# Kernel optimization log

Hardware: AMD Instinct MI355X
Metric: run time of the kernel (lower is better)

Reference implementation:

```python
import jax, jax.numpy as jnp
import numpy as np

D = 256        # node/edge feature dim
H = 256        # MLP hidden dim
NG = 80000     # grid (src) nodes
NM = 20000     # mesh (dst) nodes
E = 160000     # g2m edges
EPS = 1e-5


def _mlp(x, W1, b1, W2, b2, g, beta):
    # MeshGraphMLP with hidden_layers=1: Linear -> SiLU -> Linear -> LayerNorm
    h = jax.nn.silu(x @ W1 + b1)
    y = h @ W2 + b2
    mu = jnp.mean(y, axis=-1, keepdims=True)
    var = jnp.var(y, axis=-1, keepdims=True)
    return (y - mu) * jax.lax.rsqrt(var + EPS) * g + beta


def setup_inputs() -> dict:
    key = jax.random.key(0)
    ks = jax.random.split(key, 16)

    def rn(k, shape, s=0.02):
        return jax.random.normal(k, shape, dtype=jnp.float32) * s

    inp = {
        "g2m_efeat": jax.random.normal(ks[0], (E, D), dtype=jnp.float32),
        "grid_nfeat": jax.random.normal(ks[1], (NG, D), dtype=jnp.float32),
        "mesh_nfeat": jax.random.normal(ks[2], (NM, D), dtype=jnp.float32),
        "src_idx": jax.random.randint(ks[3], (E,), 0, NG, dtype=jnp.int32),
        "dst_idx": jax.random.randint(ks[4], (E,), 0, NM, dtype=jnp.int32),
        # edge MLP (concat variant): input = [efeat | src_feat | dst_feat] -> 3D
        "eW1": rn(ks[5], (3 * D, H)), "eb1": jnp.zeros((H,), jnp.float32),
        "eW2": rn(ks[6], (H, D)),     "eb2": jnp.zeros((D,), jnp.float32),
        "eg": jnp.ones((D,), jnp.float32), "ebeta": jnp.zeros((D,), jnp.float32),
        # src node MLP: D -> H -> D
        "sW1": rn(ks[7], (D, H)), "sb1": jnp.zeros((H,), jnp.float32),
        "sW2": rn(ks[8], (H, D)), "sb2": jnp.zeros((D,), jnp.float32),
        "sg": jnp.ones((D,), jnp.float32), "sbeta": jnp.zeros((D,), jnp.float32),
        # dst node MLP: (D_agg + D_node) = 2D -> H -> D
        "dW1": rn(ks[9], (2 * D, H)), "db1": jnp.zeros((H,), jnp.float32),
        "dW2": rn(ks[10], (H, D)),    "db2": jnp.zeros((D,), jnp.float32),
        "dg": jnp.ones((D,), jnp.float32), "dbeta": jnp.zeros((D,), jnp.float32),
    }
    return inp


def reference(g2m_efeat, grid_nfeat, mesh_nfeat, src_idx, dst_idx,
              eW1, eb1, eW2, eb2, eg, ebeta,
              sW1, sb1, sW2, sb2, sg, sbeta,
              dW1, db1, dW2, db2, dg, dbeta):
    # edge MLP: gather src/dst node features, concat with edge features
    e_in = jnp.concatenate(
        [g2m_efeat, grid_nfeat[src_idx], mesh_nfeat[dst_idx]], axis=-1)  # [E, 3D]
    efeat = _mlp(e_in, eW1, eb1, eW2, eb2, eg, ebeta)                    # [E, D]
    # aggregate_and_concat: copy_e_sum scatter to dst mesh nodes, concat node feats
    agg = jax.ops.segment_sum(efeat, dst_idx, num_segments=NM)           # [NM, D]
    cat_feat = jnp.concatenate([agg, mesh_nfeat], axis=-1)               # [NM, 2D]
    mesh_out = mesh_nfeat + _mlp(cat_feat, dW1, db1, dW2, db2, dg, dbeta)
    grid_out = grid_nfeat + _mlp(grid_nfeat, sW1, sb1, sW2, sb2, sg, sbeta)
    return (grid_out, mesh_out)
```

## Files before the change

kernel.cpp:

```cpp
#include <hip/hip_runtime.h>
#include <hip/hip_bf16.h>

#define DD 256
#define NGN 80000
#define NMN 20000
#define NEE 160000

typedef unsigned short u16;
typedef __attribute__((ext_vector_type(8))) short s16x8;
typedef __attribute__((ext_vector_type(4))) short s16x4;
typedef __attribute__((ext_vector_type(4))) float f32x4;

__device__ __forceinline__ u16 f2bf(float f) {
  union { float f; unsigned u; } v; v.f = f;
  unsigned r = (v.u + 0x7FFFu + ((v.u >> 16) & 1u)) >> 16;
  return (u16)r;
}
__device__ __forceinline__ float bf2f(u16 x) {
  union { unsigned u; float f; } v; v.u = ((unsigned)x) << 16;
  return v.f;
}

__global__ void pack_weights(const float* __restrict__ W, u16* __restrict__ dst, int K) {
  int idx = blockIdx.x * 256 + threadIdx.x;
  if (idx >= K * 256) return;
  int i = idx & 7;
  int lane = (idx >> 3) & 63;
  int nt = (idx >> 9) & 15;
  int kt = idx >> 13;
  int k = kt * 32 + 4 * (lane >> 4) + (i < 4 ? i : 12 + i);
  int n = nt * 16 + (lane & 15);
  dst[idx] = f2bf(W[(size_t)k * 256 + n]);
}

__device__ __forceinline__ void stage16k(const u16* __restrict__ gsrc, u16* lds, int tid) {
  const s16x8* s = (const s16x8*)gsrc;
  s16x8* d = (s16x8*)lds;
#pragma unroll
  for (int j = 0; j < 4; ++j) d[tid + 256 * j] = s[tid + 256 * j];
}

__global__ __launch_bounds__(256, 2) void gemm_ns(
    const float* __restrict__ X, const u16* __restrict__ Wp,
    u16* __restrict__ Y, int n) {
  __shared__ u16 bstage[8192];
  __shared__ u16 ob[16384];
  const int tid = threadIdx.x;
  const int lane = tid & 63;
  const int wave = tid >> 6;
  const int mr = wave >> 1, nc = wave & 1;
  const int g = lane >> 4, lr = lane & 15;
  const int row0 = blockIdx.x * 64;

  const float* pX[2];
#pragma unroll
  for (int mt = 0; mt < 2; ++mt) {
    int r = min(row0 + mr * 32 + mt * 16 + lr, n - 1);
    pX[mt] = X + (size_t)r * DD;
  }
  const f32x4 fz = {0.f, 0.f, 0.f, 0.f};
  f32x4 acc[2][8];
#pragma unroll
  for (int mt = 0; mt < 2; ++mt)
#pragma unroll
    for (int nt = 0; nt < 8; ++nt) acc[mt][nt] = fz;

  for (int kl = 0; kl < 8; ++kl) {
    __syncthreads();
    stage16k(Wp + (size_t)kl * 8192, bstage, tid);
    __syncthreads();
    s16x8 afr[2];
    const int c0 = kl * 32 + 4 * g;
#pragma unroll
    for (int mt = 0; mt < 2; ++mt) {
      f32x4 f0 = *(const f32x4*)(pX[mt] + c0);
      f32x4 f1 = *(const f32x4*)(pX[mt] + c0 + 16);
      s16x8 a;
#pragma unroll
      for (int j = 0; j < 4; ++j) {
        a[j] = (short)f2bf(f0[j]);
        a[4 + j] = (short)f2bf(f1[j]);
      }
      afr[mt] = a;
    }
#pragma unroll
    for (int nt = 0; nt < 8; ++nt) {
      s16x8 b = *(const s16x8*)(bstage + ((size_t)(nc * 8 + nt) * 64 + lane) * 8);
      acc[0][nt] = __builtin_amdgcn_mfma_f32_16x16x32_bf16(afr[0], b, acc[0][nt], 0, 0, 0);
      acc[1][nt] = __builtin_amdgcn_mfma_f32_16x16x32_bf16(afr[1], b, acc[1][nt], 0, 0, 0);
    }
  }
#pragma unroll
  for (int mt = 0; mt < 2; ++mt)
#pragma unroll
    for (int nt = 0; nt < 8; ++nt)
#pragma unroll
      for (int i = 0; i < 4; ++i) {
        int rowL = mr * 32 + mt * 16 + 4 * g + i;
        int col = nc * 128 + nt * 16 + lr;
        int byte = rowL * 512 + ((col * 2) ^ ((rowL & 7) << 4));
        *(u16*)((char*)ob + byte) = f2bf(acc[mt][nt][i]);
      }
  __syncthreads();
#pragma unroll
  for (int rr = 0; rr < 16; ++rr) {
    int rowL = wave * 16 + rr;
    int rg = row0 + rowL;
    if (rg < n) {
      s16x4 v = *(const s16x4*)((char*)ob + rowL * 512 + ((lane * 8) ^ ((rowL & 7) << 4)));
      *(s16x4*)(Y + (size_t)rg * DD + lane * 4) = v;
    }
  }
}

__global__ __launch_bounds__(256, 2) void edge_fused(
    const float* __restrict__ efeat,
    const u16* __restrict__ GSp, const u16* __restrict__ GMp,
    const int* __restrict__ sidx, const int* __restrict__ didx,
    const u16* __restrict__ W1p, const float* __restrict__ b1,
    const u16* __restrict__ W2p, const float* __restrict__ b2,
    const float* __restrict__ gam, const float* __restrict__ bet,
    float* __restrict__ agg) {
  __shared__ u16 uni[16384];
  __shared__ u16 bstage[8192];
  __shared__ float2 pstats[64][2];

  const int tid = threadIdx.x;
  const int lane = tid & 63;
  const int wave = tid >> 6;
  const int mr = wave >> 1, nc = wave & 1;
  const int g = lane >> 4, lr = lane & 15;
  const int row0 = blockIdx.x * 64;

#pragma unroll
  for (int j = 0; j < 8; ++j) {
    int e = wave * 16 + j * 2 + (lane >> 5);
    int rg = row0 + e;
    int rs = sidx[rg], rd = didx[rg];
    int co = (lane & 31) * 8;
    s16x8 a = *(const s16x8*)(GSp + (size_t)rs * DD + co);
    s16x8 b = *(const s16x8*)(GMp + (size_t)rd * DD + co);
    s16x8 o;
#pragma unroll
    for (int k2 = 0; k2 < 8; ++k2)
      o[k2] = (short)f2bf(bf2f((u16)a[k2]) + bf2f((u16)b[k2]));
    int byte = e * 512 + ((co * 2) ^ ((e & 7) << 4));
    *(s16x8*)((char*)uni + byte) = o;
  }
  __syncthreads();

  f32x4 acc[2][8];
#pragma unroll
  for (int mt = 0; mt < 2; ++mt)
#pragma unroll
    for (int nt = 0; nt < 8; ++nt)
#pragma unroll
      for (int i = 0; i < 4; ++i) {
        int rowL = mr * 32 + mt * 16 + 4 * g + i;
        int col = nc * 128 + nt * 16 + lr;
        int byte = rowL * 512 + ((col * 2) ^ ((rowL & 7) << 4));
        acc[mt][nt][i] = bf2f(*(const u16*)((char*)uni + byte));
      }

  const float* pe[2];
#pragma unroll
  for (int mt = 0; mt < 2; ++mt)
    pe[mt] = efeat + (size_t)(row0 + mr * 32 + mt * 16 + lr) * DD;

  for (int kl = 0; kl < 8; ++kl) {
    __syncthreads();
    stage16k(W1p + (size_t)kl * 8192, bstage, tid);
    __syncthreads();
    s16x8 afr[2];
    const int c0 = kl * 32 + 4 * g;
#pragma unroll
    for (int mt = 0; mt < 2; ++mt) {
      f32x4 f0 = *(const f32x4*)(pe[mt] + c0);
      f32x4 f1 = *(const f32x4*)(pe[mt] + c0 + 16);
      s16x8 a;
#pragma unroll
      for (int j = 0; j < 4; ++j) {
        a[j] = (short)f2bf(f0[j]);
        a[4 + j] = (short)f2bf(f1[j]);
      }
      afr[mt] = a;
    }
#pragma unroll
    for (int nt = 0; nt < 8; ++nt) {
      s16x8 b = *(const s16x8*)(bstage + ((size_t)(nc * 8 + nt) * 64 + lane) * 8);
      acc[0][nt] = __builtin_amdgcn_mfma_f32_16x16x32_bf16(afr[0], b, acc[0][nt], 0, 0, 0);
      acc[1][nt] = __builtin_amdgcn_mfma_f32_16x16x32_bf16(afr[1], b, acc[1][nt], 0, 0, 0);
    }
  }

  {
    float b1v[8];
#pragma unroll
    for (int nt = 0; nt < 8; ++nt) b1v[nt] = b1[nc * 128 + nt * 16 + lr];
#pragma unroll
    for (int mt = 0; mt < 2; ++mt)
#pragma unroll
      for (int nt = 0; nt < 8; ++nt)
#pragma unroll
        for (int i = 0; i < 4; ++i) {
          float x = acc[mt][nt][i] + b1v[nt];
          float h = x / (1.f + __expf(-x));
          int rowL = mr * 32 + mt * 16 + 4 * g + i;
          int col = nc * 128 + nt * 16 + lr;
          int byte = rowL * 512 + ((col * 2) ^ ((rowL & 7) << 4));
          *(u16*)((char*)uni + byte) = f2bf(h);
        }
  }

  f32x4 acc2[2][8];
  const f32x4 fz = {0.f, 0.f, 0.f, 0.f};
#pragma unroll
  for (int mt = 0; mt < 2; ++mt)
#pragma unroll
    for (int nt = 0; nt < 8; ++nt) acc2[mt][nt] = fz;

  for (int kt2 = 0; kt2 < 8; ++kt2) {
    __syncthreads();
    stage16k(W2p + (size_t)kt2 * 8192, bstage, tid);
    __syncthreads();
    s16x8 afr[2];
#pragma unroll
    for (int mt = 0; mt < 2; ++mt) {
      int rowL = mr * 32 + mt * 16 + lr;
      int swz = (rowL & 7) << 4;
      int cL = kt2 * 32 + 4 * g;
      s16x4 lo = *(const s16x4*)((char*)uni + rowL * 512 + ((cL * 2) ^ swz));
      s16x4 hi = *(const s16x4*)((char*)uni + rowL * 512 + (((cL + 16) * 2) ^ swz));
      s16x8 a;
#pragma unroll
      for (int j = 0; j < 4; ++j) {
        a[j] = lo[j];
        a[4 + j] = hi[j];
      }
      afr[mt] = a;
    }
#pragma unroll
    for (int nt = 0; nt < 8; ++nt) {
      s16x8 b = *(const s16x8*)(bstage + ((size_t)(nc * 8 + nt) * 64 + lane) * 8);
      acc2[0][nt] = __builtin_amdgcn_mfma_f32_16x16x32_bf16(afr[0], b, acc2[0][nt], 0, 0, 0);
      acc2[1][nt] = __builtin_amdgcn_mfma_f32_16x16x32_bf16(afr[1], b, acc2[1][nt], 0, 0, 0);
    }
  }

  float b2v[8], gv[8], bv[8];
#pragma unroll
  for (int nt = 0; nt < 8; ++nt) {
    int col = nc * 128 + nt * 16 + lr;
    b2v[nt] = b2[col];
    gv[nt] = gam[col];
    bv[nt] = bet[col];
  }
#pragma unroll
  for (int mt = 0; mt < 2; ++mt)
#pragma unroll
    for (int i = 0; i < 4; ++i) {
      float s = 0.f, s2 = 0.f;
#pragma unroll
      for (int nt = 0; nt < 8; ++nt) {
        float y = acc2[mt][nt][i] + b2v[nt];
        s += y;
        s2 += y * y;
      }
#pragma unroll
      for (int m = 1; m < 16; m <<= 1) {
        s += __shfl_xor(s, m);
        s2 += __shfl_xor(s2, m);
      }
      if (lr == 0) pstats[mr * 32 + mt * 16 + 4 * g + i][nc] = make_float2(s, s2);
    }
  __syncthreads();
#pragma unroll
  for (int mt = 0; mt < 2; ++mt)
#pragma unroll
    for (int i = 0; i < 4; ++i) {
      int rowL = mr * 32 + mt * 16 + 4 * g + i;
      float2 pa = pstats[rowL][0], pb = pstats[rowL][1];
      float sum = pa.x + pb.x, sq = pa.y + pb.y;
      float mu = sum * (1.f / 256.f);
      float var = fmaxf(sq * (1.f / 256.f) - mu * mu, 0.f);
      float rs = rsqrtf(var + 1e-5f);
      int rg = row0 + rowL;
      int dn = didx[rg];
#pragma unroll
      for (int nt = 0; nt < 8; ++nt) {
        int col = nc * 128 + nt * 16 + lr;
        float y = acc2[mt][nt][i] + b2v[nt];
        float val = (y - mu) * rs * gv[nt] + bv[nt];
        atomicAdd(agg + (size_t)dn * DD + col, val);
      }
    }
}

template <int MODE, int K1>
__global__ __launch_bounds__(256, 2) void mlp_fused(
    const float* __restrict__ xa, const float* __restrict__ xb,
    const u16* __restrict__ W1p, const float* __restrict__ b1,
    const u16* __restrict__ W2p, const float* __restrict__ b2,
    const float* __restrict__ gam, const float* __restrict__ bet,
    const float* __restrict__ resid, float* __restrict__ out, int nrows) {
  __shared__ u16 bstage[8192];
  __shared__ u16 hbuf[64 * 256];
  __shared__ float2 pstats[64][2];

  const int tid = threadIdx.x;
  const int lane = tid & 63;
  const int wave = tid >> 6;
  const int mr = wave >> 1, nc = wave & 1;
  const int g = lane >> 4, lr = lane & 15;
  const int row0 = blockIdx.x * 64;

  const float* pA[2][2];
#pragma unroll
  for (int mt = 0; mt < 2; ++mt) {
    int r = row0 + mr * 32 + mt * 16 + lr;
    if (MODE == 2) r = min(r, nrows - 1);
    pA[mt][0] = xa + (size_t)r * DD;
    if constexpr (MODE == 2) pA[mt][1] = xb + (size_t)r * DD;
  }

  const f32x4 fz = {0.f, 0.f, 0.f, 0.f};
  f32x4 acc[2][8];
#pragma unroll
  for (int mt = 0; mt < 2; ++mt)
#pragma unroll
    for (int nt = 0; nt < 8; ++nt) acc[mt][nt] = fz;

#pragma unroll
  for (int region = 0; region < K1 / 256; ++region) {
    for (int kl = 0; kl < 8; ++kl) {
      const int kt = region * 8 + kl;
      __syncthreads();
      stage16k(W1p + (size_t)kt * 8192, bstage, tid);
      __syncthreads();
      s16x8 afr[2];
      const int c0 = kl * 32 + 4 * g;
#pragma unroll
      for (int mt = 0; mt < 2; ++mt) {
        const float* p = pA[mt][region] + c0;
        f32x4 f0 = *(const f32x4*)p;
        f32x4 f1 = *(const f32x4*)(p + 16);
        s16x8 a;
#pragma unroll
        for (int j = 0; j < 4; ++j) {
          a[j] = (short)f2bf(f0[j]);
          a[4 + j] = (short)f2bf(f1[j]);
        }
        afr[mt] = a;
      }
#pragma unroll
      for (int nt = 0; nt < 8; ++nt) {
        s16x8 b = *(const s16x8*)(bstage + ((size_t)(nc * 8 + nt) * 64 + lane) * 8);
        acc[0][nt] = __builtin_amdgcn_mfma_f32_16x16x32_bf16(afr[0], b, acc[0][nt], 0, 0, 0);
        acc[1][nt] = __builtin_amdgcn_mfma_f32_16x16x32_bf16(afr[1], b, acc[1][nt], 0, 0, 0);
      }
    }
  }

  {
    float b1v[8];
#pragma unroll
    for (int nt = 0; nt < 8; ++nt) b1v[nt] = b1[nc * 128 + nt * 16 + lr];
#pragma unroll
    for (int mt = 0; mt < 2; ++mt)
#pragma unroll
      for (int nt = 0; nt < 8; ++nt)
#pragma unroll
        for (int i = 0; i < 4; ++i) {
          float x = acc[mt][nt][i] + b1v[nt];
          float h = x / (1.f + __expf(-x));
          int rowL = mr * 32 + mt * 16 + 4 * g + i;
          int col = nc * 128 + nt * 16 + lr;
          int byte = rowL * 512 + ((col * 2) ^ ((rowL & 7) << 4));
          *(u16*)((char*)hbuf + byte) = f2bf(h);
        }
  }

  f32x4 acc2[2][8];
#pragma unroll
  for (int mt = 0; mt < 2; ++mt)
#pragma unroll
    for (int nt = 0; nt < 8; ++nt) acc2[mt][nt] = fz;

  for (int kt2 = 0; kt2 < 8; ++kt2) {
    __syncthreads();
    stage16k(W2p + (size_t)kt2 * 8192, bstage, tid);
    __syncthreads();
    s16x8 afr[2];
#pragma unroll
    for (int mt = 0; mt < 2; ++mt) {
      int rowL = mr * 32 + mt * 16 + lr;
      int swz = (rowL & 7) << 4;
      int cL = kt2 * 32 + 4 * g;
      s16x4 lo = *(const s16x4*)((char*)hbuf + rowL * 512 + ((cL * 2) ^ swz));
      s16x4 hi = *(const s16x4*)((char*)hbuf + rowL * 512 + (((cL + 16) * 2) ^ swz));
      s16x8 a;
#pragma unroll
      for (int j = 0; j < 4; ++j) {
        a[j] = lo[j];
        a[4 + j] = hi[j];
      }
      afr[mt] = a;
    }
#pragma unroll
    for (int nt = 0; nt < 8; ++nt) {
      s16x8 b = *(const s16x8*)(bstage + ((size_t)(nc * 8 + nt) * 64 + lane) * 8);
      acc2[0][nt] = __builtin_amdgcn_mfma_f32_16x16x32_bf16(afr[0], b, acc2[0][nt], 0, 0, 0);
      acc2[1][nt] = __builtin_amdgcn_mfma_f32_16x16x32_bf16(afr[1], b, acc2[1][nt], 0, 0, 0);
    }
  }

  float b2v[8], gv[8], bv[8];
#pragma unroll
  for (int nt = 0; nt < 8; ++nt) {
    int col = nc * 128 + nt * 16 + lr;
    b2v[nt] = b2[col];
    gv[nt] = gam[col];
    bv[nt] = bet[col];
  }
#pragma unroll
  for (int mt = 0; mt < 2; ++mt)
#pragma unroll
    for (int i = 0; i < 4; ++i) {
      float s = 0.f, s2 = 0.f;
#pragma unroll
      for (int nt = 0; nt < 8; ++nt) {
        float y = acc2[mt][nt][i] + b2v[nt];
        s += y;
        s2 += y * y;
      }
#pragma unroll
      for (int m = 1; m < 16; m <<= 1) {
        s += __shfl_xor(s, m);
        s2 += __shfl_xor(s2, m);
      }
      if (lr == 0) pstats[mr * 32 + mt * 16 + 4 * g + i][nc] = make_float2(s, s2);
    }
  __syncthreads();
#pragma unroll
  for (int mt = 0; mt < 2; ++mt)
#pragma unroll
    for (int i = 0; i < 4; ++i) {
      int rowL = mr * 32 + mt * 16 + 4 * g + i;
      float2 pa = pstats[rowL][0], pb = pstats[rowL][1];
      float sum = pa.x + pb.x, sq = pa.y + pb.y;
      float mu = sum * (1.f / 256.f);
      float var = fmaxf(sq * (1.f / 256.f) - mu * mu, 0.f);
      float rs = rsqrtf(var + 1e-5f);
      int rg = row0 + rowL;
      if (MODE == 2 && rg >= nrows) continue;
#pragma unroll
      for (int nt = 0; nt < 8; ++nt) {
        int col = nc * 128 + nt * 16 + lr;
        float y = acc2[mt][nt][i] + b2v[nt];
        float val = (y - mu) * rs * gv[nt] + bv[nt];
        out[(size_t)rg * DD + col] = resid[(size_t)rg * DD + col] + val;
      }
    }
}

extern "C" void kernel_launch(void* const* d_in, const int* in_sizes, int n_in,
                              void* d_out, int out_size, void* d_ws, size_t ws_size,
                              hipStream_t stream) {
  const float* g2m  = (const float*)d_in[0];
  const float* grid = (const float*)d_in[1];
  const float* mesh = (const float*)d_in[2];
  const int* sidx = (const int*)d_in[3];
  const int* didx = (const int*)d_in[4];
  const float* eW1 = (const float*)d_in[5];
  const float* eb1 = (const float*)d_in[6];
  const float* eW2 = (const float*)d_in[7];
  const float* eb2 = (const float*)d_in[8];
  const float* eg  = (const float*)d_in[9];
  const float* ebt = (const float*)d_in[10];
  const float* sW1 = (const float*)d_in[11];
  const float* sb1 = (const float*)d_in[12];
  const float* sW2 = (const float*)d_in[13];
  const float* sb2 = (const float*)d_in[14];
  const float* sg  = (const float*)d_in[15];
  const float* sbt = (const float*)d_in[16];
  const float* dW1 = (const float*)d_in[17];
  const float* db1 = (const float*)d_in[18];
  const float* dW2 = (const float*)d_in[19];
  const float* db2 = (const float*)d_in[20];
  const float* dg  = (const float*)d_in[21];
  const float* dbt = (const float*)d_in[22];

  float* agg = (float*)d_ws;
  u16* wp = (u16*)((char*)d_ws + (size_t)NMN * DD * 4);
  u16* eW1p = wp;
  u16* eW2p = eW1p + 768 * 256;
  u16* sW1p = eW2p + 256 * 256;
  u16* sW2p = sW1p + 256 * 256;
  u16* dW1p = sW2p + 256 * 256;
  u16* dW2p = dW1p + 512 * 256;

  float* gout = (float*)d_out;
  float* mout = gout + (size_t)NGN * DD;
  u16* GSp = (u16*)d_out;
  u16* GMp = GSp + (size_t)NGN * DD;

  (void)hipMemsetAsync(agg, 0, (size_t)NMN * DD * 4, stream);
  pack_weights<<<768, 256, 0, stream>>>(eW1, eW1p, 768);
  pack_weights<<<256, 256, 0, stream>>>(eW2, eW2p, 256);
  pack_weights<<<256, 256, 0, stream>>>(sW1, sW1p, 256);
  pack_weights<<<256, 256, 0, stream>>>(sW2, sW2p, 256);
  pack_weights<<<512, 256, 0, stream>>>(dW1, dW1p, 512);
  pack_weights<<<256, 256, 0, stream>>>(dW2, dW2p, 256);

  gemm_ns<<<NGN / 64, 256, 0, stream>>>(grid, eW1p + 8 * 8192, GSp, NGN);
  gemm_ns<<<(NMN + 63) / 64, 256, 0, stream>>>(mesh, eW1p + 16 * 8192, GMp, NMN);

  edge_fused<<<NEE / 64, 256, 0, stream>>>(
      g2m, GSp, GMp, sidx, didx, eW1p, eb1, eW2p, eb2, eg, ebt, agg);

  mlp_fused<2, 512><<<(NMN + 63) / 64, 256, 0, stream>>>(
      agg, mesh, dW1p, db1, dW2p, db2, dg, dbt, mesh, mout, NMN);
  mlp_fused<1, 256><<<NGN / 64, 256, 0, stream>>>(
      grid, nullptr, sW1p, sb1, sW2p, sb2, sg, sbt, grid, gout, NGN);
}
```

Baseline: 446.9 us.

## Sort edges by destination via CSR and segment-reduce before atomics; drop weight LDS staging

Builds a destination-sorted edge permutation (histogram, scan, fill) so each edge block processes edges grouped by destination and reduces consecutive same-destination rows in LDS before issuing one atomicAdd per run, instead of one atomic per edge element. Weight B-fragments are now read directly from global memory rather than staged through LDS with per-k barriers. The A operands are staged once into swizzled LDS as bf16, and launch bounds rise to 4 blocks per CU. The trade-offs are three extra small kernels, the gather of efeat through the permutation, and B traffic that now depends on cache hits.

```diff
diff --git a/kernel.cpp b/kernel.cpp
--- a/kernel.cpp
+++ b/kernel.cpp
@@ -33,18 +33,50 @@
   dst[idx] = f2bf(W[(size_t)k * 256 + n]);
 }
 
-__device__ __forceinline__ void stage16k(const u16* __restrict__ gsrc, u16* lds, int tid) {
-  const s16x8* s = (const s16x8*)gsrc;
-  s16x8* d = (s16x8*)lds;
-#pragma unroll
-  for (int j = 0; j < 4; ++j) d[tid + 256 * j] = s[tid + 256 * j];
-}
-
-__global__ __launch_bounds__(256, 2) void gemm_ns(
+__global__ void csr_hist(const int* __restrict__ didx, int* __restrict__ cnt) {
+  int i = blockIdx.x * 256 + threadIdx.x;
+  if (i < NEE) atomicAdd(cnt + didx[i], 1);
+}
+__global__ void csr_scan(const int* __restrict__ cnt, int* __restrict__ cursor) {
+  __shared__ int psum[256];
+  const int CH = (NMN + 255) / 256;
+  int t = threadIdx.x;
+  int base = t * CH, s = 0;
+  for (int k = 0; k < CH; ++k) { int i = base + k; if (i < NMN) s += cnt[i]; }
+  psum[t] = s;
+  __syncthreads();
+  for (int off = 1; off < 256; off <<= 1) {
+    int v = (t >= off) ? psum[t - off] : 0;
+    __syncthreads();
+    psum[t] += v;
+    __syncthreads();
+  }
+  int run = psum[t] - s;
+  for (int k = 0; k < CH; ++k) {
+    int i = base + k;
+    if (i < NMN) { cursor[i] = run; run += cnt[i]; }
+  }
+}
+__global__ void csr_fill(const int* __restrict__ didx, int* __restrict__ cursor,
+                         int* __restrict__ eids) {
+  int e = blockIdx.x * 256 + threadIdx.x;
+  if (e < NEE) { int p = atomicAdd(cursor + didx[e], 1); eids[p] = e; }
+}
+
+__device__ __forceinline__ s16x8 ldsA(const u16* uni, int rowL, int cL) {
+  int swz = (rowL & 7) << 4;
+  s16x4 lo = *(const s16x4*)((const char*)uni + rowL * 512 + ((cL * 2) ^ swz));
+  s16x4 hi = *(const s16x4*)((const char*)uni + rowL * 512 + (((cL + 16) * 2) ^ swz));
+  s16x8 a;
+#pragma unroll
+  for (int j = 0; j < 4; ++j) { a[j] = lo[j]; a[4 + j] = hi[j]; }
+  return a;
+}
+
+__global__ __launch_bounds__(256, 4) void gemm_ns(
     const float* __restrict__ X, const u16* __restrict__ Wp,
     u16* __restrict__ Y, int n) {
-  __shared__ u16 bstage[8192];
-  __shared__ u16 ob[16384];
+  __shared__ u16 uni[16384];
   const int tid = threadIdx.x;
   const int lane = tid & 63;
   const int wave = tid >> 6;
@@ -52,12 +84,21 @@
   const int g = lane >> 4, lr = lane & 15;
   const int row0 = blockIdx.x * 64;
 
-  const float* pX[2];
-#pragma unroll
-  for (int mt = 0; mt < 2; ++mt) {
-    int r = min(row0 + mr * 32 + mt * 16 + lr, n - 1);
-    pX[mt] = X + (size_t)r * DD;
-  }
+#pragma unroll
+  for (int j = 0; j < 8; ++j) {
+    int e = wave * 16 + j * 2 + (lane >> 5);
+    int r = min(row0 + e, n - 1);
+    const float* src = X + (size_t)r * DD + (lane & 31) * 8;
+    f32x4 f0 = *(const f32x4*)src;
+    f32x4 f1 = *(const f32x4*)(src + 4);
+    s16x8 o;
+#pragma unroll
+    for (int k = 0; k < 4; ++k) { o[k] = (short)f2bf(f0[k]); o[4 + k] = (short)f2bf(f1[k]); }
+    int co = (lane & 31) * 8;
+    *(s16x8*)((char*)uni + e * 512 + ((co * 2) ^ ((e & 7) << 4))) = o;
+  }
+  __syncthreads();
+
   const f32x4 fz = {0.f, 0.f, 0.f, 0.f};
   f32x4 acc[2][8];
 #pragma unroll
@@ -66,30 +107,23 @@
     for (int nt = 0; nt < 8; ++nt) acc[mt][nt] = fz;
 
   for (int kl = 0; kl < 8; ++kl) {
-    __syncthreads();
-    stage16k(Wp + (size_t)kl * 8192, bstage, tid);
-    __syncthreads();
     s16x8 afr[2];
-    const int c0 = kl * 32 + 4 * g;
-#pragma unroll
-    for (int mt = 0; mt < 2; ++mt) {
-      f32x4 f0 = *(const f32x4*)(pX[mt] + c0);
-      f32x4 f1 = *(const f32x4*)(pX[mt] + c0 + 16);
-      s16x8 a;
-#pragma unroll
-      for (int j = 0; j < 4; ++j) {
-        a[j] = (short)f2bf(f0[j]);
-        a[4 + j] = (short)f2bf(f1[j]);
-      }
-      afr[mt] = a;
-    }
-#pragma unroll
-    for (int nt = 0; nt < 8; ++nt) {
-      s16x8 b = *(const s16x8*)(bstage + ((size_t)(nc * 8 + nt) * 64 + lane) * 8);
-      acc[0][nt] = __builtin_amdgcn_mfma_f32_16x16x32_bf16(afr[0], b, acc[0][nt], 0, 0, 0);
-      acc[1][nt] = __builtin_amdgcn_mfma_f32_16x16x32_bf16(afr[1], b, acc[1][nt], 0, 0, 0);
-    }
-  }
+#pragma unroll
+    for (int mt = 0; mt < 2; ++mt) afr[mt] = ldsA(uni, mr * 32 + mt * 16 + lr, kl * 32 + 4 * g);
+#pragma unroll
+    for (int h = 0; h < 2; ++h) {
+      s16x8 bfr[4];
+#pragma unroll
+      for (int q = 0; q < 4; ++q)
+        bfr[q] = *(const s16x8*)(Wp + (size_t)kl * 8192 + ((nc * 8 + h * 4 + q) * 64 + lane) * 8);
+#pragma unroll
+      for (int q = 0; q < 4; ++q) {
+        acc[0][h * 4 + q] = __builtin_amdgcn_mfma_f32_16x16x32_bf16(afr[0], bfr[q], acc[0][h * 4 + q], 0, 0, 0);
+        acc[1][h * 4 + q] = __builtin_amdgcn_mfma_f32_16x16x32_bf16(afr[1], bfr[q], acc[1][h * 4 + q], 0, 0, 0);
+      }
+    }
+  }
+  __syncthreads();
 #pragma unroll
   for (int mt = 0; mt < 2; ++mt)
 #pragma unroll
@@ -98,8 +132,7 @@
       for (int i = 0; i < 4; ++i) {
         int rowL = mr * 32 + mt * 16 + 4 * g + i;
         int col = nc * 128 + nt * 16 + lr;
-        int byte = rowL * 512 + ((col * 2) ^ ((rowL & 7) << 4));
-        *(u16*)((char*)ob + byte) = f2bf(acc[mt][nt][i]);
+        *(u16*)((char*)uni + rowL * 512 + ((col * 2) ^ ((rowL & 7) << 4))) = f2bf(acc[mt][nt][i]);
       }
   __syncthreads();
 #pragma unroll
@@ -107,23 +140,25 @@
     int rowL = wave * 16 + rr;
     int rg = row0 + rowL;
     if (rg < n) {
-      s16x4 v = *(const s16x4*)((char*)ob + rowL * 512 + ((lane * 8) ^ ((rowL & 7) << 4)));
+      s16x4 v = *(const s16x4*)((char*)uni + rowL * 512 + ((lane * 8) ^ ((rowL & 7) << 4)));
       *(s16x4*)(Y + (size_t)rg * DD + lane * 4) = v;
     }
   }
 }
 
-__global__ __launch_bounds__(256, 2) void edge_fused(
+__global__ __launch_bounds__(256, 4) void edge_fused(
     const float* __restrict__ efeat,
     const u16* __restrict__ GSp, const u16* __restrict__ GMp,
-    const int* __restrict__ sidx, const int* __restrict__ didx,
+    const int* __restrict__ sidx, const int* __restrict__ eids,
     const u16* __restrict__ W1p, const float* __restrict__ b1,
     const u16* __restrict__ W2p, const float* __restrict__ b2,
     const float* __restrict__ gam, const float* __restrict__ bet,
-    float* __restrict__ agg) {
+    const int* __restrict__ didx, float* __restrict__ agg) {
   __shared__ u16 uni[16384];
-  __shared__ u16 bstage[8192];
   __shared__ float2 pstats[64][2];
+  __shared__ int eidL[64];
+  __shared__ int srcL[64];
+  __shared__ int dstL[64];
 
   const int tid = threadIdx.x;
   const int lane = tid & 63;
@@ -132,20 +167,24 @@
   const int g = lane >> 4, lr = lane & 15;
   const int row0 = blockIdx.x * 64;
 
+  if (tid < 64) {
+    int e = eids[row0 + tid];
+    eidL[tid] = e;
+    srcL[tid] = sidx[e];
+    dstL[tid] = didx[e];
+  }
+  __syncthreads();
+
 #pragma unroll
   for (int j = 0; j < 8; ++j) {
     int e = wave * 16 + j * 2 + (lane >> 5);
-    int rg = row0 + e;
-    int rs = sidx[rg], rd = didx[rg];
     int co = (lane & 31) * 8;
-    s16x8 a = *(const s16x8*)(GSp + (size_t)rs * DD + co);
-    s16x8 b = *(const s16x8*)(GMp + (size_t)rd * DD + co);
+    s16x8 a = *(const s16x8*)(GSp + (size_t)srcL[e] * DD + co);
+    s16x8 b = *(const s16x8*)(GMp + (size_t)dstL[e] * DD + co);
     s16x8 o;
 #pragma unroll
-    for (int k2 = 0; k2 < 8; ++k2)
-      o[k2] = (short)f2bf(bf2f((u16)a[k2]) + bf2f((u16)b[k2]));
-    int byte = e * 512 + ((co * 2) ^ ((e & 7) << 4));
-    *(s16x8*)((char*)uni + byte) = o;
+    for (int k = 0; k < 8; ++k) o[k] = (short)f2bf(bf2f((u16)a[k]) + bf2f((u16)b[k]));
+    *(s16x8*)((char*)uni + e * 512 + ((co * 2) ^ ((e & 7) << 4))) = o;
   }
   __syncthreads();
 
@@ -158,40 +197,42 @@
       for (int i = 0; i < 4; ++i) {
         int rowL = mr * 32 + mt * 16 + 4 * g + i;
         int col = nc * 128 + nt * 16 + lr;
-        int byte = rowL * 512 + ((col * 2) ^ ((rowL & 7) << 4));
-        acc[mt][nt][i] = bf2f(*(const u16*)((char*)uni + byte));
-      }
-
-  const float* pe[2];
-#pragma unroll
-  for (int mt = 0; mt < 2; ++mt)
-    pe[mt] = efeat + (size_t)(row0 + mr * 32 + mt * 16 + lr) * DD;
+        acc[mt][nt][i] = bf2f(*(const u16*)((char*)uni + rowL * 512 + ((col * 2) ^ ((rowL & 7) << 4))));
+      }
+  __syncthreads();
+
+#pragma unroll
+  for (int j = 0; j < 8; ++j) {
+    int e = wave * 16 + j * 2 + (lane >> 5);
+    const float* src = efeat + (size_t)eidL[e] * DD + (lane & 31) * 8;
+    f32x4 f0 = *(const f32x4*)src;
+    f32x4 f1 = *(const f32x4*)(src + 4);
+    s16x8 o;
+#pragma unroll
+    for (int k = 0; k < 4; ++k) { o[k] = (short)f2bf(f0[k]); o[4 + k] = (short)f2bf(f1[k]); }
+    int co = (lane & 31) * 8;
+    *(s16x8*)((char*)uni + e * 512 + ((co * 2) ^ ((e & 7) << 4))) = o;
+  }
+  __syncthreads();
 
   for (int kl = 0; kl < 8; ++kl) {
-    __syncthreads();
-    stage16k(W1p + (size_t)kl * 8192, bstage, tid);
-    __syncthreads();
     s16x8 afr[2];
-    const int c0 = kl * 32 + 4 * g;
-#pragma unroll
-    for (int mt = 0; mt < 2; ++mt) {
-      f32x4 f0 = *(const f32x4*)(pe[mt] + c0);
-      f32x4 f1 = *(const f32x4*)(pe[mt] + c0 + 16);
-      s16x8 a;
-#pragma unroll
-      for (int j = 0; j < 4; ++j) {
-        a[j] = (short)f2bf(f0[j]);
-        a[4 + j] = (short)f2bf(f1[j]);
-      }
-      afr[mt] = a;
-    }
-#pragma unroll
-    for (int nt = 0; nt < 8; ++nt) {
-      s16x8 b = *(const s16x8*)(bstage + ((size_t)(nc * 8 + nt) * 64 + lane) * 8);
-      acc[0][nt] = __builtin_amdgcn_mfma_f32_16x16x32_bf16(afr[0], b, acc[0][nt], 0, 0, 0);
-      acc[1][nt] = __builtin_amdgcn_mfma_f32_16x16x32_bf16(afr[1], b, acc[1][nt], 0, 0, 0);
-    }
-  }
+#pragma unroll
+    for (int mt = 0; mt < 2; ++mt) afr[mt] = ldsA(uni, mr * 32 + mt * 16 + lr, kl * 32 + 4 * g);
+#pragma unroll
+    for (int h = 0; h < 2; ++h) {
+      s16x8 bfr[4];
+#pragma unroll
+      for (int q = 0; q < 4; ++q)
+        bfr[q] = *(const s16x8*)(W1p + (size_t)kl * 8192 + ((nc * 8 + h * 4 + q) * 64 + lane) * 8);
+#pragma unroll
+      for (int q = 0; q < 4; ++q) {
+        acc[0][h * 4 + q] = __builtin_amdgcn_mfma_f32_16x16x32_bf16(afr[0], bfr[q], acc[0][h * 4 + q], 0, 0, 0);
+        acc[1][h * 4 + q] = __builtin_amdgcn_mfma_f32_16x16x32_bf16(afr[1], bfr[q], acc[1][h * 4 + q], 0, 0, 0);
+      }
+    }
+  }
+  __syncthreads();
 
   {
     float b1v[8];
@@ -207,10 +248,10 @@
           float h = x / (1.f + __expf(-x));
           int rowL = mr * 32 + mt * 16 + 4 * g + i;
           int col = nc * 128 + nt * 16 + lr;
-          int byte = rowL * 512 + ((col * 2) ^ ((rowL & 7) << 4));
-          *(u16*)((char*)uni + byte) = f2bf(h);
+          *(u16*)((char*)uni + rowL * 512 + ((col * 2) ^ ((rowL & 7) << 4))) = f2bf(h);
         }
   }
+  __syncthreads();
 
   f32x4 acc2[2][8];
   const f32x4 fz = {0.f, 0.f, 0.f, 0.f};
@@ -218,32 +259,21 @@
   for (int mt = 0; mt < 2; ++mt)
 #pragma unroll
     for (int nt = 0; nt < 8; ++nt) acc2[mt][nt] = fz;
-
-  for (int kt2 = 0; kt2 < 8; ++kt2) {
-    __syncthreads();
-    stage16k(W2p + (size_t)kt2 * 8192, bstage, tid);
-    __syncthreads();
+  for (int kl = 0; kl < 8; ++kl) {
     s16x8 afr[2];
 #pragma unroll
-    for (int mt = 0; mt < 2; ++mt) {
-      int rowL = mr * 32 + mt * 16 + lr;
-      int swz = (rowL & 7) << 4;
-      int cL = kt2 * 32 + 4 * g;
-      s16x4 lo = *(const s16x4*)((char*)uni + rowL * 512 + ((cL * 2) ^ swz));
-      s16x4 hi = *(const s16x4*)((char*)uni + rowL * 512 + (((cL + 16) * 2) ^ swz));
-      s16x8 a;
-#pragma unroll
-      for (int j = 0; j < 4; ++j) {
-        a[j] = lo[j];
-        a[4 + j] = hi[j];
-      }
-      afr[mt] = a;
-    }
-#pragma unroll
-    for (int nt = 0; nt < 8; ++nt) {
-      s16x8 b = *(const s16x8*)(bstage + ((size_t)(nc * 8 + nt) * 64 + lane) * 8);
-      acc2[0][nt] = __builtin_amdgcn_mfma_f32_16x16x32_bf16(afr[0], b, acc2[0][nt], 0, 0, 0);
-      acc2[1][nt] = __builtin_amdgcn_mfma_f32_16x16x32_bf16(afr[1], b, acc2[1][nt], 0, 0, 0);
+    for (int mt = 0; mt < 2; ++mt) afr[mt] = ldsA(uni, mr * 32 + mt * 16 + lr, kl * 32 + 4 * g);
+#pragma unroll
+    for (int h = 0; h < 2; ++h) {
+      s16x8 bfr[4];
+#pragma unroll
+      for (int q = 0; q < 4; ++q)
+        bfr[q] = *(const s16x8*)(W2p + (size_t)kl * 8192 + ((nc * 8 + h * 4 + q) * 64 + lane) * 8);
+#pragma unroll
+      for (int q = 0; q < 4; ++q) {
+        acc2[0][h * 4 + q] = __builtin_amdgcn_mfma_f32_16x16x32_bf16(afr[0], bfr[q], acc2[0][h * 4 + q], 0, 0, 0);
+        acc2[1][h * 4 + q] = __builtin_amdgcn_mfma_f32_16x16x32_bf16(afr[1], bfr[q], acc2[1][h * 4 + q], 0, 0, 0);
+      }
     }
   }
 
@@ -274,6 +304,7 @@
       if (lr == 0) pstats[mr * 32 + mt * 16 + 4 * g + i][nc] = make_float2(s, s2);
     }
   __syncthreads();
+
 #pragma unroll
   for (int mt = 0; mt < 2; ++mt)
 #pragma unroll
@@ -284,27 +315,42 @@
       float mu = sum * (1.f / 256.f);
       float var = fmaxf(sq * (1.f / 256.f) - mu * mu, 0.f);
       float rs = rsqrtf(var + 1e-5f);
-      int rg = row0 + rowL;
-      int dn = didx[rg];
 #pragma unroll
       for (int nt = 0; nt < 8; ++nt) {
         int col = nc * 128 + nt * 16 + lr;
         float y = acc2[mt][nt][i] + b2v[nt];
         float val = (y - mu) * rs * gv[nt] + bv[nt];
-        atomicAdd(agg + (size_t)dn * DD + col, val);
-      }
-    }
+        *(u16*)((char*)uni + rowL * 512 + ((col * 2) ^ ((rowL & 7) << 4))) = f2bf(val);
+      }
+    }
+  __syncthreads();
+
+  {
+    int c = tid;
+    float sum = 0.f;
+    int prev = dstL[0];
+#pragma unroll 8
+    for (int r = 0; r < 64; ++r) {
+      int d = dstL[r];
+      if (d != prev) {
+        atomicAdd(agg + (size_t)prev * DD + c, sum);
+        sum = 0.f;
+        prev = d;
+      }
+      sum += bf2f(*(const u16*)((char*)uni + r * 512 + ((c * 2) ^ ((r & 7) << 4))));
+    }
+    atomicAdd(agg + (size_t)prev * DD + c, sum);
+  }
 }
 
 template <int MODE, int K1>
-__global__ __launch_bounds__(256, 2) void mlp_fused(
+__global__ __launch_bounds__(256, 4) void mlp_fused(
     const float* __restrict__ xa, const float* __restrict__ xb,
     const u16* __restrict__ W1p, const float* __restrict__ b1,
     const u16* __restrict__ W2p, const float* __restrict__ b2,
     const float* __restrict__ gam, const float* __restrict__ bet,
     const float* __restrict__ resid, float* __restrict__ out, int nrows) {
-  __shared__ u16 bstage[8192];
-  __shared__ u16 hbuf[64 * 256];
+  __shared__ u16 uni[16384];
   __shared__ float2 pstats[64][2];
 
   const int tid = threadIdx.x;
@@ -314,15 +360,6 @@
   const int g = lane >> 4, lr = lane & 15;
   const int row0 = blockIdx.x * 64;
 
-  const float* pA[2][2];
-#pragma unroll
-  for (int mt = 0; mt < 2; ++mt) {
-    int r = row0 + mr * 32 + mt * 16 + lr;
-    if (MODE == 2) r = min(r, nrows - 1);
-    pA[mt][0] = xa + (size_t)r * DD;
-    if constexpr (MODE == 2) pA[mt][1] = xb + (size_t)r * DD;
-  }
-
   const f32x4 fz = {0.f, 0.f, 0.f, 0.f};
   f32x4 acc[2][8];
 #pragma unroll
@@ -332,34 +369,42 @@
 
 #pragma unroll
   for (int region = 0; region < K1 / 256; ++region) {
+    __syncthreads();
+    const float* Xr = (region == 0) ? xa : xb;
+#pragma unroll
+    for (int j = 0; j < 8; ++j) {
+      int e = wave * 16 + j * 2 + (lane >> 5);
+      int r = min(row0 + e, nrows - 1);
+      const float* src = Xr + (size_t)r * DD + (lane & 31) * 8;
+      f32x4 f0 = *(const f32x4*)src;
+      f32x4 f1 = *(const f32x4*)(src + 4);
+      s16x8 o;
+#pragma unroll
+      for (int k = 0; k < 4; ++k) { o[k] = (short)f2bf(f0[k]); o[4 + k] = (short)f2bf(f1[k]); }
+      int co = (lane & 31) * 8;
+      *(s16x8*)((char*)uni + e * 512 + ((co * 2) ^ ((e & 7) << 4))) = o;
+    }
+    __syncthreads();
     for (int kl = 0; kl < 8; ++kl) {
       const int kt = region * 8 + kl;
-      __syncthreads();
-      stage16k(W1p + (size_t)kt * 8192, bstage, tid);
-      __syncthreads();
       s16x8 afr[2];
-      const int c0 = kl * 32 + 4 * g;
-#pragma unroll
-      for (int mt = 0; mt < 2; ++mt) {
-        const float* p = pA[mt][region] + c0;
-        f32x4 f0 = *(const f32x4*)p;
-        f32x4 f1 = *(const f32x4*)(p + 16);
-        s16x8 a;
-#pragma unroll
-        for (int j = 0; j < 4; ++j) {
-          a[j] = (short)f2bf(f0[j]);
-          a[4 + j] = (short)f2bf(f1[j]);
+#pragma unroll
+      for (int mt = 0; mt < 2; ++mt) afr[mt] = ldsA(uni, mr * 32 + mt * 16 + lr, kl * 32 + 4 * g);
+#pragma unroll
+      for (int h = 0; h < 2; ++h) {
+        s16x8 bfr[4];
+#pragma unroll
+        for (int q = 0; q < 4; ++q)
+          bfr[q] = *(const s16x8*)(W1p + (size_t)kt * 8192 + ((nc * 8 + h * 4 + q) * 64 + lane) * 8);
+#pragma unroll
+        for (int q = 0; q < 4; ++q) {
+          acc[0][h * 4 + q] = __builtin_amdgcn_mfma_f32_16x16x32_bf16(afr[0], bfr[q], acc[0][h * 4 + q], 0, 0, 0);
+          acc[1][h * 4 + q] = __builtin_amdgcn_mfma_f32_16x16x32_bf16(afr[1], bfr[q], acc[1][h * 4 + q], 0, 0, 0);
         }
-        afr[mt] = a;
-      }
-#pragma unroll
-      for (int nt = 0; nt < 8; ++nt) {
-        s16x8 b = *(const s16x8*)(bstage + ((size_t)(nc * 8 + nt) * 64 + lane) * 8);
-        acc[0][nt] = __builtin_amdgcn_mfma_f32_16x16x32_bf16(afr[0], b, acc[0][nt], 0, 0, 0);
-        acc[1][nt] = __builtin_amdgcn_mfma_f32_16x16x32_bf16(afr[1], b, acc[1][nt], 0, 0, 0);
-      }
-    }
-  }
+      }
+    }
+  }
+  __syncthreads();
 
   {
     float b1v[8];
@@ -375,42 +420,31 @@
           float h = x / (1.f + __expf(-x));
           int rowL = mr * 32 + mt * 16 + 4 * g + i;
           int col = nc * 128 + nt * 16 + lr;
-          int byte = rowL * 512 + ((col * 2) ^ ((rowL & 7) << 4));
-          *(u16*)((char*)hbuf + byte) = f2bf(h);
+          *(u16*)((char*)uni + rowL * 512 + ((col * 2) ^ ((rowL & 7) << 4))) = f2bf(h);
         }
   }
+  __syncthreads();
 
   f32x4 acc2[2][8];
 #pragma unroll
   for (int mt = 0; mt < 2; ++mt)
 #pragma unroll
     for (int nt = 0; nt < 8; ++nt) acc2[mt][nt] = fz;
-
-  for (int kt2 = 0; kt2 < 8; ++kt2) {
-    __syncthreads();
-    stage16k(W2p + (size_t)kt2 * 8192, bstage, tid);
-    __syncthreads();
+  for (int kl = 0; kl < 8; ++kl) {
     s16x8 afr[2];
 #pragma unroll
-    for (int mt = 0; mt < 2; ++mt) {
-      int rowL = mr * 32 + mt * 16 + lr;
-      int swz = (rowL & 7) << 4;
-      int cL = kt2 * 32 + 4 * g;
-      s16x4 lo = *(const s16x4*)((char*)hbuf + rowL * 512 + ((cL * 2) ^ swz));
-      s16x4 hi = *(const s16x4*)((char*)hbuf + rowL * 512 + (((cL + 16) * 2) ^ swz));
-      s16x8 a;
-#pragma unroll
-      for (int j = 0; j < 4; ++j) {
-        a[j] = lo[j];
-        a[4 + j] = hi[j];
-      }
-      afr[mt] = a;
-    }
-#pragma unroll
-    for (int nt = 0; nt < 8; ++nt) {
-      s16x8 b = *(const s16x8*)(bstage + ((size_t)(nc * 8 + nt) * 64 + lane) * 8);
-      acc2[0][nt] = __builtin_amdgcn_mfma_f32_16x16x32_bf16(afr[0], b, acc2[0][nt], 0, 0, 0);
-      acc2[1][nt] = __builtin_amdgcn_mfma_f32_16x16x32_bf16(afr[1], b, acc2[1][nt], 0, 0, 0);
+    for (int mt = 0; mt < 2; ++mt) afr[mt] = ldsA(uni, mr * 32 + mt * 16 + lr, kl * 32 + 4 * g);
+#pragma unroll
+    for (int h = 0; h < 2; ++h) {
+      s16x8 bfr[4];
+#pragma unroll
+      for (int q = 0; q < 4; ++q)
+        bfr[q] = *(const s16x8*)(W2p + (size_t)kl * 8192 + ((nc * 8 + h * 4 + q) * 64 + lane) * 8);
+#pragma unroll
+      for (int q = 0; q < 4; ++q) {
+        acc2[0][h * 4 + q] = __builtin_amdgcn_mfma_f32_16x16x32_bf16(afr[0], bfr[q], acc2[0][h * 4 + q], 0, 0, 0);
+        acc2[1][h * 4 + q] = __builtin_amdgcn_mfma_f32_16x16x32_bf16(afr[1], bfr[q], acc2[1][h * 4 + q], 0, 0, 0);
+      }
     }
   }
 
@@ -490,8 +524,13 @@
   const float* dg  = (const float*)d_in[21];
   const float* dbt = (const float*)d_in[22];
 
-  float* agg = (float*)d_ws;
-  u16* wp = (u16*)((char*)d_ws + (size_t)NMN * DD * 4);
+  char* w = (char*)d_ws;
+  float* agg = (float*)w;
+  u16* wp = (u16*)(w + 20480000);
+  int* cnt = (int*)(w + 20480000 + 1179648);
+  int* cursor = cnt + 20480;
+  int* eids = cursor + 20480;
+
   u16* eW1p = wp;
   u16* eW2p = eW1p + 768 * 256;
   u16* sW1p = eW2p + 256 * 256;
@@ -504,7 +543,9 @@
   u16* GSp = (u16*)d_out;
   u16* GMp = GSp + (size_t)NGN * DD;
 
-  (void)hipMemsetAsync(agg, 0, (size_t)NMN * DD * 4, stream);
+  (void)hipMemsetAsync(agg, 0, 20480000, stream);
+  (void)hipMemsetAsync(cnt, 0, 81920, stream);
+
   pack_weights<<<768, 256, 0, stream>>>(eW1, eW1p, 768);
   pack_weights<<<256, 256, 0, stream>>>(eW2, eW2p, 256);
   pack_weights<<<256, 256, 0, stream>>>(sW1, sW1p, 256);
@@ -512,11 +553,15 @@
   pack_weights<<<512, 256, 0, stream>>>(dW1, dW1p, 512);
   pack_weights<<<256, 256, 0, stream>>>(dW2, dW2p, 256);
 
+  csr_hist<<<(NEE + 255) / 256, 256, 0, stream>>>(didx, cnt);
+  csr_scan<<<1, 256, 0, stream>>>(cnt, cursor);
+  csr_fill<<<(NEE + 255) / 256, 256, 0, stream>>>(didx, cursor, eids);
+
   gemm_ns<<<NGN / 64, 256, 0, stream>>>(grid, eW1p + 8 * 8192, GSp, NGN);
   gemm_ns<<<(NMN + 63) / 64, 256, 0, stream>>>(mesh, eW1p + 16 * 8192, GMp, NMN);
 
   edge_fused<<<NEE / 64, 256, 0, stream>>>(
-      g2m, GSp, GMp, sidx, didx, eW1p, eb1, eW2p, eb2, eg, ebt, agg);
+      g2m, GSp, GMp, sidx, eids, eW1p, eb1, eW2p, eb2, eg, ebt, didx, agg);
 
   mlp_fused<2, 512><<<(NMN + 63) / 64, 256, 0, stream>>>(
       agg, mesh, dW1p, db1, dW2p, db2, dg, dbt, mesh, mout, NMN);
```

After: 648.5 us. +45.1%, slower.
